# Performance work log

Measured on AMD Instinct MI355X. Metric: run time of the kernel, lower is better.

Reference implementation:

```python
import jax, jax.numpy as jnp
import numpy as np

B, S, HS = 2, 2048, 4096
NH, NKV = 32, 32
HD = HS // NH
INTER = 11008
VOCAB = 32000
EPS = 1e-6
ROPE_BASE = 10000.0


def setup_inputs() -> dict:
    key = jax.random.key(0)
    ks = jax.random.split(key, 16)
    sc = 0.02
    return {
        "hidden_states": jax.random.normal(ks[0], (B, S, HS), jnp.float32),
        "input_ids": jax.random.randint(ks[1], (B, S), 0, VOCAB, jnp.int32),
        "position_ids": jnp.arange(S, dtype=jnp.int32)[None, :],
        "embed": jax.random.normal(ks[2], (VOCAB, HS), jnp.float32) * sc,
        "fc_w": jax.random.normal(ks[3], (HS, 2 * HS), jnp.float32) * sc,
        "fc_b": jnp.zeros((HS,), jnp.float32),
        "q_w": jax.random.normal(ks[4], (NH * HD, HS), jnp.float32) * sc,
        "k_w": jax.random.normal(ks[5], (NKV * HD, HS), jnp.float32) * sc,
        "v_w": jax.random.normal(ks[6], (NKV * HD, HS), jnp.float32) * sc,
        "o_w": jax.random.normal(ks[7], (HS, NH * HD), jnp.float32) * sc,
        "gate_w": jax.random.normal(ks[8], (INTER, HS), jnp.float32) * sc,
        "up_w": jax.random.normal(ks[9], (INTER, HS), jnp.float32) * sc,
        "down_w": jax.random.normal(ks[10], (HS, INTER), jnp.float32) * sc,
        "post_ln_w": jnp.ones((HS,), jnp.float32),
    }


def _rotate_half(x):
    x1, x2 = jnp.split(x, 2, axis=-1)
    return jnp.concatenate((-x2, x1), axis=-1)


def _rms_norm(x, w, eps=EPS):
    x32 = x.astype(jnp.float32)
    x32 = x32 * jax.lax.rsqrt(jnp.mean(x32 * x32, axis=-1, keepdims=True) + eps)
    return (w * x32).astype(x.dtype)


def _forward(hidden_states, input_ids, position_ids, embed, fc_w, fc_b,
             q_w, k_w, v_w, o_w, gate_w, up_w, down_w, post_ln_w):
    # Embedding lookup (detached in original via no_grad)
    embeds = jax.lax.stop_gradient(embed[input_ids])  # [B,S,HS]
    h = jnp.concatenate((embeds, hidden_states), axis=-1) @ fc_w.T + fc_b  # [B,S,HS]

    # --- decoder layer 0 (no input_layernorm) ---
    residual = h
    q = (h @ q_w.T).reshape(B, S, NH, HD).transpose(0, 2, 1, 3)   # [B,NH,S,HD]
    k = (h @ k_w.T).reshape(B, S, NKV, HD).transpose(0, 2, 1, 3)
    v = (h @ v_w.T).reshape(B, S, NKV, HD).transpose(0, 2, 1, 3)

    # RoPE
    pos = position_ids[0].astype(jnp.float32)                      # [S]
    inv_freq = 1.0 / (ROPE_BASE ** (jnp.arange(0, HD, 2, dtype=jnp.float32) / HD))
    freqs = pos[:, None] * inv_freq[None, :]                       # [S,HD/2]
    emb = jnp.concatenate((freqs, freqs), axis=-1)                 # [S,HD]
    cos = jnp.cos(emb)[None, None, :, :]
    sin = jnp.sin(emb)[None, None, :, :]
    q = q * cos + _rotate_half(q) * sin
    k = k * cos + _rotate_half(k) * sin

    # attention (num_kv_groups == 1 here)
    scores = jnp.einsum('bhqd,bhkd->bhqk', q, k) / np.sqrt(HD)     # [B,NH,S,S]
    causal = jnp.triu(jnp.ones((S, S), bool), 1)
    scores = jnp.where(causal[None, None], -jnp.inf, scores)
    attn = jax.nn.softmax(scores.astype(jnp.float32), axis=-1).astype(q.dtype)
    out = jnp.einsum('bhqk,bhkd->bhqd', attn, v)                   # [B,NH,S,HD]
    out = out.transpose(0, 2, 1, 3).reshape(B, S, HS)
    attn_out = out @ o_w.T

    h = residual + attn_out
    residual = h
    hn = _rms_norm(h, post_ln_w)
    mlp = (jax.nn.silu(hn @ gate_w.T) * (hn @ up_w.T)) @ down_w.T
    return residual + mlp


def reference(hidden_states, input_ids, position_ids, embed, fc_w, fc_b,
              q_w, k_w, v_w, o_w, gate_w, up_w, down_w, post_ln_w):
    return _forward(hidden_states, input_ids, position_ids, embed, fc_w, fc_b,
                    q_w, k_w, v_w, o_w, gate_w, up_w, down_w, post_ln_w)
```

## Files before the change

kernel.cpp:

```cpp
#include <hip/hip_runtime.h>
#include <hip/hip_bf16.h>

typedef __attribute__((ext_vector_type(8))) short short8;
typedef __attribute__((ext_vector_type(4))) short short4v;
typedef __attribute__((ext_vector_type(4))) float floatx4;

#define B_SZ 2
#define S_SZ 2048
#define HS_SZ 4096
#define NH_SZ 32
#define HD_SZ 128
#define INTER_SZ 11008
#define M_TOT 4096

__device__ __forceinline__ float b2f(short s){
  unsigned int u = ((unsigned int)(unsigned short)s) << 16;
  return __builtin_bit_cast(float, u);
}
__device__ __forceinline__ short f2b(float f){
  unsigned int u = __builtin_bit_cast(unsigned int, f);
  u = (u + 0x7FFFu + ((u >> 16) & 1u)) >> 16;
  return (short)u;
}

typedef __attribute__((address_space(1))) const unsigned int gu32;
typedef __attribute__((address_space(3))) unsigned int lu32;
__device__ __forceinline__ void gl2lds16(const short* g, short* l){
  __builtin_amdgcn_global_load_lds((gu32*)g, (lu32*)l, 16, 0, 0);
}

#define BARRIER() asm volatile("s_barrier" ::: "memory")
#define WAITV8()  asm volatile("s_waitcnt vmcnt(8)" ::: "memory")
#define WAITV4()  asm volatile("s_waitcnt vmcnt(4)" ::: "memory")
#define WAITV0()  asm volatile("s_waitcnt vmcnt(0)" ::: "memory")

__global__ void cvt_bf16_kernel(const float* __restrict__ src, short* __restrict__ dst, long n8){
  long idx = (long)blockIdx.x * blockDim.x + threadIdx.x;
  if (idx >= n8) return;
  long e = idx * 8;
  floatx4 v0 = *(const floatx4*)(src + e);
  floatx4 v1 = *(const floatx4*)(src + e + 4);
  short8 o;
  o[0]=f2b(v0[0]); o[1]=f2b(v0[1]); o[2]=f2b(v0[2]); o[3]=f2b(v0[3]);
  o[4]=f2b(v1[0]); o[5]=f2b(v1[1]); o[6]=f2b(v1[2]); o[7]=f2b(v1[3]);
  *(short8*)(dst + e) = o;
}

__global__ void embed_concat_kernel(const float* __restrict__ hidden,
                                    const int* __restrict__ ids,
                                    const float* __restrict__ embed,
                                    short* __restrict__ X0){
  long idx = (long)blockIdx.x * blockDim.x + threadIdx.x;
  const long total = (long)M_TOT * (2*HS_SZ) / 4;
  if (idx >= total) return;
  long e = idx * 4;
  int m = (int)(e / (2*HS_SZ));
  int c = (int)(e % (2*HS_SZ));
  const float* src;
  if (c < HS_SZ){
    src = embed + (long)ids[m]*HS_SZ + c;
  } else {
    src = hidden + (long)m*HS_SZ + (c - HS_SZ);
  }
  floatx4 v = *(const floatx4*)src;
  short4v o;
  o[0]=f2b(v[0]); o[1]=f2b(v[1]); o[2]=f2b(v[2]); o[3]=f2b(v[3]);
  *(short4v*)(X0 + e) = o;
}

template<int EPI>
__global__ __launch_bounds__(512, 2)
void gemm256_kernel(const short* __restrict__ A, const short* __restrict__ Bw,
                    int M, int N, int K,
                    const float* __restrict__ bias,
                    const float* __restrict__ resid,
                    short* __restrict__ Cbf,
                    float* __restrict__ Cf){
  __shared__ __align__(16) short lds[65536];
  const int tid = threadIdx.x;
  const int wid = tid >> 6;
  const int lane = tid & 63;
  const int wr = wid >> 2, wc = wid & 3;
  const int lr = lane & 15, lk = lane >> 4;

  const int nwg = gridDim.x * gridDim.y;
  const int id  = blockIdx.y * gridDim.x + blockIdx.x;
  const int cpx = nwg >> 3;
  const int sw  = (id & 7) * cpx + (id >> 3);
  const int bx  = sw % gridDim.x;
  const int by  = sw / gridDim.x;
  const int m0 = bx * 256, n0 = by * 256;

  const int srow = wid*16 + (lane >> 2);
  const int scol = (lane & 3) * 8;
  const short* ga0 = A  + (long)(m0 + srow)*K + scol;
  const short* ga1 = A  + (long)(m0 + 128 + srow)*K + scol;
  const short* gb0 = Bw + (long)(n0 + srow)*K + scol;
  const short* gb1 = Bw + (long)(n0 + 128 + srow)*K + scol;

  floatx4 acc[8][4] = {};
  const int nt = K >> 5;

  auto stage = [&](int t){
    const long kk = (long)t * 32;
    short* db = lds + ((t & 3) * 16384) + wid*512;
    gl2lds16(ga0 + kk, db);
    gl2lds16(ga1 + kk, db + 4096);
    gl2lds16(gb0 + kk, db + 8192);
    gl2lds16(gb1 + kk, db + 12288);
  };

  stage(0); stage(1); stage(2);

  for (int t = 0; t < nt; ++t){
    if (t + 3 < nt) stage(t + 3);
    if (t + 2 < nt)      { WAITV8(); }
    else if (t + 1 < nt) { WAITV4(); }
    else                 { WAITV0(); }
    BARRIER();
    const short* sb = lds + (t & 3) * 16384;
    short8 bfr[4], af[8];
    #pragma unroll
    for (int j=0;j<4;j++) bfr[j] = *(const short8*)(sb + 8192 + (wc*64 + j*16 + lr)*32 + lk*8);
    #pragma unroll
    for (int i=0;i<8;i++) af[i]  = *(const short8*)(sb + (wr*128 + i*16 + lr)*32 + lk*8);
    __builtin_amdgcn_s_setprio(1);
    #pragma unroll
    for (int i=0;i<8;i++)
      #pragma unroll
      for (int j=0;j<4;j++)
        acc[i][j] = __builtin_amdgcn_mfma_f32_16x16x32_bf16(af[i], bfr[j], acc[i][j], 0,0,0);
    __builtin_amdgcn_s_setprio(0);
    BARRIER();
  }

  #pragma unroll
  for (int mf=0; mf<8; mf++){
    #pragma unroll
    for (int nf=0; nf<4; nf++){
      const int col = n0 + wc*64 + nf*16 + lr;
      float bcol = (EPI==1) ? bias[col] : 0.0f;
      #pragma unroll
      for (int r=0; r<4; r++){
        const int row = m0 + wr*128 + mf*16 + lk*4 + r;
        float v = acc[mf][nf][r] + bcol;
        if (EPI==2) v += resid[(long)row*N + col];
        if (EPI==0 || EPI==1) Cbf[(long)row*N + col] = f2b(v);
        if (EPI==1 || EPI==2) Cf[(long)row*N + col] = v;
      }
    }
  }
}

__global__ void rope_kernel(short* __restrict__ q, short* __restrict__ k,
                            const int* __restrict__ pos_ids){
  long idx = (long)blockIdx.x * blockDim.x + threadIdx.x;
  const long total = (long)M_TOT * NH_SZ * (HD_SZ/2);
  if (idx >= total) return;
  int i  = (int)(idx & 63);
  long rh = idx >> 6;
  int h  = (int)(rh & 31);
  int m  = (int)(rh >> 5);
  int s  = m & (S_SZ - 1);
  float p = (float)pos_ids[s];
  const float L2_10000 = 13.28771237954945f;
  float inv = exp2f(-(2.0f*i/(float)HD_SZ) * L2_10000);
  float fr = p * inv;
  float sn, cs;
  sincosf(fr, &sn, &cs);
  long base = (long)m*HS_SZ + h*HD_SZ;
  short* qp = q + base;
  short* kp = k + base;
  float q1=b2f(qp[i]), q2=b2f(qp[i+64]);
  qp[i]    = f2b(q1*cs - q2*sn);
  qp[i+64] = f2b(q2*cs + q1*sn);
  float k1=b2f(kp[i]), k2=b2f(kp[i+64]);
  kp[i]    = f2b(k1*cs - k2*sn);
  kp[i+64] = f2b(k2*cs + k1*sn);
}

__global__ __launch_bounds__(256)
void vtrans_kernel(const short* __restrict__ V, short* __restrict__ VT){
  __shared__ short tile[64][68];
  const int s0 = blockIdx.x * 64;
  const int d0 = blockIdx.y * 64;
  const int bh = blockIdx.z;
  const int b = bh >> 5, h = bh & 31;
  const int tid = threadIdx.x;
  #pragma unroll
  for (int it=0; it<2; it++){
    int e = (it*256 + tid) * 8;
    int ss = e >> 6, col = e & 63;
    short8 v = *(const short8*)(V + ((long)(b*S_SZ + s0 + ss))*HS_SZ + h*HD_SZ + d0 + col);
    #pragma unroll
    for (int j=0;j<8;j++) tile[ss][col+j] = v[j];
  }
  __syncthreads();
  #pragma unroll
  for (int it=0; it<2; it++){
    int e = (it*256 + tid) * 8;
    int dd = e >> 6, scol = e & 63;
    short8 w;
    #pragma unroll
    for (int j=0;j<8;j++) w[j] = tile[scol+j][dd];
    *(short8*)(VT + ((long)(bh*HD_SZ + d0 + dd))*S_SZ + s0 + scol) = w;
  }
}

__global__ __launch_bounds__(256,2)
void attn_kernel(const short* __restrict__ Q, const short* __restrict__ K,
                 const short* __restrict__ VT, short* __restrict__ O){
  constexpr int LPD = 72;
  __shared__ __align__(16) short lds[32768];
  __shared__ __align__(16) short p_lds[4][16*LPD];
  const int bh = blockIdx.y;
  const int b = bh >> 5, h = bh & 31;
  const int q0 = blockIdx.x * 64;
  const int tid = threadIdx.x, wid = tid>>6, lane = tid&63;
  const int lr = lane & 15, lk = lane >> 4;
  const float scale = 0.08838834764831845f;

  const short* qbase = Q + ((long)(b*S_SZ + q0 + wid*16))*HS_SZ + h*HD_SZ;
  short8 qf[4];
  #pragma unroll
  for (int t=0;t<4;t++)
    qf[t] = *(const short8*)(qbase + (long)lr*HS_SZ + t*32 + lk*8);

  const short* kb[4]; const short* vb[4];
  int kloff[4], vloff[4];
  #pragma unroll
  for (int p=0;p<4;p++){
    const int seg = wid*4 + p;
    const int rowk = seg*4 + (lane >> 4);
    const int slotk = (lane & 15) ^ (rowk & 15);
    kb[p] = K + ((long)(b*S_SZ) + rowk)*HS_SZ + h*HD_SZ + slotk*8;
    kloff[p] = seg*512;
    const int dv = seg*8 + (lane >> 3);
    const int slotv = (lane & 7) ^ (dv & 7);
    vb[p] = VT + ((long)(bh*HD_SZ + dv))*S_SZ + slotv*8;
    vloff[p] = 8192 + seg*512;
  }

  floatx4 oacc[8] = {};
  float m_run[4] = {-1e30f,-1e30f,-1e30f,-1e30f};
  float l_run[4] = {0.f,0.f,0.f,0.f};

  const int nt = blockIdx.x + 1;

  #pragma unroll
  for (int p=0;p<4;p++){
    gl2lds16(kb[p], lds + kloff[p]);
    gl2lds16(vb[p], lds + vloff[p]);
  }

  for (int t=0; t<nt; ++t){
    const int dbase = (t & 1) * 16384;
    const int nbase = ((t+1) & 1) * 16384;
    if (t+1 < nt){
      const long kkn = (long)(t+1)*64*HS_SZ;
      const long vkn = (long)(t+1)*64;
      #pragma unroll
      for (int p=0;p<4;p++){
        gl2lds16(kb[p] + kkn, lds + nbase + kloff[p]);
        gl2lds16(vb[p] + vkn, lds + nbase + vloff[p]);
      }
      WAITV8();
    } else {
      WAITV0();
    }
    BARRIER();
    const int kv0 = t*64;
    floatx4 sfr[4];
    #pragma unroll
    for (int fn=0; fn<4; fn++){
      floatx4 s = {0.f,0.f,0.f,0.f};
      const int row = fn*16 + lr;
      #pragma unroll
      for (int tq=0; tq<4; tq++){
        short8 kf = *(const short8*)(lds + dbase + row*128 + (((tq*4+lk)^lr)&15)*8);
        s = __builtin_amdgcn_mfma_f32_16x16x32_bf16(qf[tq], kf, s, 0,0,0);
      }
      sfr[fn] = s;
    }
    float pv[4][4];
    #pragma unroll
    for (int fn=0; fn<4; fn++){
      const int col = kv0 + fn*16 + lr;
      #pragma unroll
      for (int r=0;r<4;r++){
        const int row = q0 + wid*16 + lk*4 + r;
        float sv = sfr[fn][r] * scale;
        pv[fn][r] = (col > row) ? -1e30f : sv;
      }
    }
    float mr4[4];
    int small = 1;
    #pragma unroll
    for (int r=0;r<4;r++){
      float mr = fmaxf(fmaxf(pv[0][r], pv[1][r]), fmaxf(pv[2][r], pv[3][r]));
      mr = fmaxf(mr, __shfl_xor(mr, 1, 16));
      mr = fmaxf(mr, __shfl_xor(mr, 2, 16));
      mr = fmaxf(mr, __shfl_xor(mr, 4, 16));
      mr = fmaxf(mr, __shfl_xor(mr, 8, 16));
      mr4[r] = mr;
      small &= (mr <= m_run[r] + 8.0f) ? 1 : 0;
    }
    const int skip = __all(small);
    float alpha_[4];
    #pragma unroll
    for (int r=0;r<4;r++){
      float mnew = skip ? m_run[r] : fmaxf(m_run[r], mr4[r]);
      alpha_[r] = skip ? 1.0f : __expf(m_run[r] - mnew);
      m_run[r] = mnew;
      float rs = 0.f;
      #pragma unroll
      for (int fn=0; fn<4; fn++){
        float e = __expf(pv[fn][r] - mnew);
        p_lds[wid][(lk*4+r)*LPD + fn*16 + lr] = f2b(e);
        rs += e;
      }
      rs += __shfl_xor(rs, 1, 16);
      rs += __shfl_xor(rs, 2, 16);
      rs += __shfl_xor(rs, 4, 16);
      rs += __shfl_xor(rs, 8, 16);
      l_run[r] = l_run[r]*alpha_[r] + rs;
    }
    if (!skip){
      #pragma unroll
      for (int f=0; f<8; f++){
        #pragma unroll
        for (int r=0;r<4;r++) oacc[f][r] *= alpha_[r];
      }
    }
    short8 pf[2];
    #pragma unroll
    for (int tp=0; tp<2; tp++)
      pf[tp] = *(const short8*)(&p_lds[wid][lr*LPD + tp*32 + lk*8]);
    #pragma unroll
    for (int f=0; f<8; f++){
      const int vrow = f*16 + lr;
      #pragma unroll
      for (int tp=0; tp<2; tp++){
        short8 vf = *(const short8*)(lds + dbase + 8192 + vrow*64 + (((tp*4+lk)^(lr&7))&7)*8);
        oacc[f] = __builtin_amdgcn_mfma_f32_16x16x32_bf16(pf[tp], vf, oacc[f], 0,0,0);
      }
    }
    BARRIER();
  }
  #pragma unroll
  for (int r=0;r<4;r++){
    const float inv = 1.0f / l_run[r];
    const long row = (long)(b*S_SZ + q0 + wid*16 + lk*4 + r);
    #pragma unroll
    for (int f=0; f<8; f++){
      O[row*HS_SZ + h*HD_SZ + f*16 + lr] = f2b(oacc[f][r]*inv);
    }
  }
}

__global__ void rmsnorm_kernel(const float* __restrict__ X, const float* __restrict__ W,
                               short* __restrict__ Y){
  const int row = blockIdx.x;
  const float* x = X + (long)row*HS_SZ;
  float ss = 0.f;
  for (int c = threadIdx.x*4; c < HS_SZ; c += 256*4){
    floatx4 v = *(const floatx4*)(x + c);
    ss += v[0]*v[0] + v[1]*v[1] + v[2]*v[2] + v[3]*v[3];
  }
  ss += __shfl_xor(ss, 32); ss += __shfl_xor(ss, 16);
  ss += __shfl_xor(ss, 8);  ss += __shfl_xor(ss, 4);
  ss += __shfl_xor(ss, 2);  ss += __shfl_xor(ss, 1);
  __shared__ float red[4];
  if ((threadIdx.x & 63) == 0) red[threadIdx.x >> 6] = ss;
  __syncthreads();
  ss = red[0] + red[1] + red[2] + red[3];
  const float rs = rsqrtf(ss / (float)HS_SZ + 1e-6f);
  for (int c = threadIdx.x*4; c < HS_SZ; c += 256*4){
    floatx4 v = *(const floatx4*)(x + c);
    floatx4 w = *(const floatx4*)(W + c);
    short4v o;
    o[0]=f2b(v[0]*rs*w[0]); o[1]=f2b(v[1]*rs*w[1]);
    o[2]=f2b(v[2]*rs*w[2]); o[3]=f2b(v[3]*rs*w[3]);
    *(short4v*)(Y + (long)row*HS_SZ + c) = o;
  }
}

__global__ void silu_mul_kernel(short* __restrict__ G, const short* __restrict__ U){
  long idx = (long)blockIdx.x * blockDim.x + threadIdx.x;
  const long total = (long)M_TOT * INTER_SZ / 8;
  if (idx >= total) return;
  long e = idx * 8;
  short8 g = *(short8*)(G + e);
  short8 u = *(const short8*)(U + e);
  short8 o;
  #pragma unroll
  for (int j=0;j<8;j++){
    float gf = b2f(g[j]);
    float uf = b2f(u[j]);
    float s = gf / (1.0f + __expf(-gf));
    o[j] = f2b(s * uf);
  }
  *(short8*)(G + e) = o;
}

extern "C" void kernel_launch(void* const* d_in, const int* in_sizes, int n_in,
                              void* d_out, int out_size, void* d_ws, size_t ws_size,
                              hipStream_t stream){
  (void)in_sizes; (void)n_in; (void)out_size;
  const float* hidden = (const float*)d_in[0];
  const int*   ids    = (const int*)d_in[1];
  const int*   pos    = (const int*)d_in[2];
  const float* embed  = (const float*)d_in[3];
  const float* fc_w   = (const float*)d_in[4];
  const float* fc_b   = (const float*)d_in[5];
  const float* q_w    = (const float*)d_in[6];
  const float* k_w    = (const float*)d_in[7];
  const float* v_w    = (const float*)d_in[8];
  const float* o_w    = (const float*)d_in[9];
  const float* gate_w = (const float*)d_in[10];
  const float* up_w   = (const float*)d_in[11];
  const float* down_w = (const float*)d_in[12];
  const float* ln_w   = (const float*)d_in[13];

  char* ws = (char*)d_ws;
  size_t off = 0;
  auto alloc = [&](size_t bytes)->char*{
    char* p = ws + off;
    off = (off + bytes + 255) & ~(size_t)255;
    return p;
  };
  short* wbf  = (short*)alloc((size_t)INTER_SZ*HS_SZ*2);
  short* X0   = (short*)alloc((size_t)M_TOT*2*HS_SZ*2);
  short* h_bf = (short*)alloc((size_t)M_TOT*HS_SZ*2);
  float* h_f  = (float*)alloc((size_t)M_TOT*HS_SZ*4);
  short* q_bf = (short*)alloc((size_t)M_TOT*HS_SZ*2);
  short* k_bf = (short*)alloc((size_t)M_TOT*HS_SZ*2);
  short* v_bf = (short*)alloc((size_t)M_TOT*HS_SZ*2);
  short* vt_bf= (short*)alloc((size_t)M_TOT*HS_SZ*2);
  short* a_bf = (short*)alloc((size_t)M_TOT*HS_SZ*2);
  float* h2_f = (float*)alloc((size_t)M_TOT*HS_SZ*4);
  short* hn_bf= (short*)alloc((size_t)M_TOT*HS_SZ*2);
  short* g_bf = (short*)alloc((size_t)M_TOT*INTER_SZ*2);
  short* u_bf = (short*)alloc((size_t)M_TOT*INTER_SZ*2);
  if (ws_size < off) return;

  auto cvt = [&](const float* src, short* dst, long n){
    long n8 = n / 8;
    cvt_bf16_kernel<<<(int)((n8 + 255)/256), 256, 0, stream>>>(src, dst, n8);
  };

  embed_concat_kernel<<<32768, 256, 0, stream>>>(hidden, ids, embed, X0);

  cvt(fc_w, wbf, (long)HS_SZ*2*HS_SZ);
  gemm256_kernel<1><<<dim3(16,16), 512, 0, stream>>>(X0, wbf, M_TOT, HS_SZ, 2*HS_SZ,
                                                     fc_b, nullptr, h_bf, h_f);
  cvt(q_w, wbf, (long)HS_SZ*HS_SZ);
  gemm256_kernel<0><<<dim3(16,16), 512, 0, stream>>>(h_bf, wbf, M_TOT, HS_SZ, HS_SZ,
                                                     nullptr, nullptr, q_bf, nullptr);
  cvt(k_w, wbf, (long)HS_SZ*HS_SZ);
  gemm256_kernel<0><<<dim3(16,16), 512, 0, stream>>>(h_bf, wbf, M_TOT, HS_SZ, HS_SZ,
                                                     nullptr, nullptr, k_bf, nullptr);
  cvt(v_w, wbf, (long)HS_SZ*HS_SZ);
  gemm256_kernel<0><<<dim3(16,16), 512, 0, stream>>>(h_bf, wbf, M_TOT, HS_SZ, HS_SZ,
                                                     nullptr, nullptr, v_bf, nullptr);
  rope_kernel<<<32768, 256, 0, stream>>>(q_bf, k_bf, pos);
  vtrans_kernel<<<dim3(S_SZ/64, HD_SZ/64, B_SZ*NH_SZ), 256, 0, stream>>>(v_bf, vt_bf);
  attn_kernel<<<dim3(S_SZ/64, B_SZ*NH_SZ), 256, 0, stream>>>(q_bf, k_bf, vt_bf, a_bf);
  cvt(o_w, wbf, (long)HS_SZ*HS_SZ);
  gemm256_kernel<2><<<dim3(16,16), 512, 0, stream>>>(a_bf, wbf, M_TOT, HS_SZ, HS_SZ,
                                                     nullptr, h_f, nullptr, h2_f);
  rmsnorm_kernel<<<M_TOT, 256, 0, stream>>>(h2_f, ln_w, hn_bf);
  cvt(gate_w, wbf, (long)INTER_SZ*HS_SZ);
  gemm256_kernel<0><<<dim3(16,43), 512, 0, stream>>>(hn_bf, wbf, M_TOT, INTER_SZ, HS_SZ,
                                                     nullptr, nullptr, g_bf, nullptr);
  cvt(up_w, wbf, (long)INTER_SZ*HS_SZ);
  gemm256_kernel<0><<<dim3(16,43), 512, 0, stream>>>(hn_bf, wbf, M_TOT, INTER_SZ, HS_SZ,
                                                     nullptr, nullptr, u_bf, nullptr);
  silu_mul_kernel<<<22016, 256, 0, stream>>>(g_bf, u_bf);
  cvt(down_w, wbf, (long)HS_SZ*INTER_SZ);
  gemm256_kernel<2><<<dim3(16,16), 512, 0, stream>>>(g_bf, wbf, M_TOT, HS_SZ, INTER_SZ,
                                                     nullptr, h2_f, nullptr, (float*)d_out);
}
```

Measured before the change: 2.689 ms.

## Restructure GEMM mainloop into 8-wave ping-pong with K=64 tiles and swizzled LDS

Rewrites the 256x256 bf16 GEMM main loop to use K=64 tiles with double buffering, split into four 128x128 quadrants. Each quadrant's MFMA block is interleaved with a global-to-LDS stage of the next tile, with barriers in between. LDS rows are XOR-swizzled to avoid bank conflicts on the 64-wide rows. The aim is to overlap memory loads with MFMA work and cut LDS conflicts, at the cost of more barriers and tighter vmcnt bookkeeping that could break correctness or stall waves.

```diff
diff --git a/kernel.cpp b/kernel.cpp
--- a/kernel.cpp
+++ b/kernel.cpp
@@ -32,6 +32,7 @@
 #define BARRIER() asm volatile("s_barrier" ::: "memory")
 #define WAITV8()  asm volatile("s_waitcnt vmcnt(8)" ::: "memory")
 #define WAITV4()  asm volatile("s_waitcnt vmcnt(4)" ::: "memory")
+#define WAITV2()  asm volatile("s_waitcnt vmcnt(2)" ::: "memory")
 #define WAITV0()  asm volatile("s_waitcnt vmcnt(0)" ::: "memory")
 
 __global__ void cvt_bf16_kernel(const float* __restrict__ src, short* __restrict__ dst, long n8){
@@ -68,6 +69,35 @@
   *(short4v*)(X0 + e) = o;
 }
 
+#define G_STAGE(op,h,kof,qb) { \
+  gl2lds16(gs[op][h] + (kof), lds + (qb) + (op)*16384 + (h)*8192 + wid*1024); \
+  gl2lds16(gs[op][h] + k8 + (kof), lds + (qb) + (op)*16384 + (h)*8192 + wid*1024 + 512); }
+
+#define LD_A(Mh,pb) { \
+  _Pragma("unroll") \
+  for (int mf=0; mf<4; mf++) \
+    _Pragma("unroll") \
+    for (int ks=0; ks<2; ks++) \
+      af[mf][ks] = *(const short8*)(lds + (pb) + ((Mh)*128 + wr2*64 + mf*16 + lr)*64 + (((ks*4+lk)^lr7))*8); }
+
+#define LD_B(BB,Nh,pb) { \
+  _Pragma("unroll") \
+  for (int nf=0; nf<2; nf++) \
+    _Pragma("unroll") \
+    for (int ks=0; ks<2; ks++) \
+      BB[nf][ks] = *(const short8*)(lds + (pb) + 16384 + ((Nh)*128 + wc2*32 + nf*16 + lr)*64 + (((ks*4+lk)^lr7))*8); }
+
+#define MMQ(Mh,Nh,BB) { \
+  __builtin_amdgcn_s_setprio(1); \
+  _Pragma("unroll") \
+  for (int mf=0; mf<4; mf++) \
+    _Pragma("unroll") \
+    for (int nf=0; nf<2; nf++){ \
+      acc[Mh][Nh][mf][nf] = __builtin_amdgcn_mfma_f32_16x16x32_bf16(af[mf][0], BB[nf][0], acc[Mh][Nh][mf][nf], 0,0,0); \
+      acc[Mh][Nh][mf][nf] = __builtin_amdgcn_mfma_f32_16x16x32_bf16(af[mf][1], BB[nf][1], acc[Mh][Nh][mf][nf], 0,0,0); \
+    } \
+  __builtin_amdgcn_s_setprio(0); }
+
 template<int EPI>
 __global__ __launch_bounds__(512, 2)
 void gemm256_kernel(const short* __restrict__ A, const short* __restrict__ Bw,
@@ -80,8 +110,9 @@
   const int tid = threadIdx.x;
   const int wid = tid >> 6;
   const int lane = tid & 63;
-  const int wr = wid >> 2, wc = wid & 3;
+  const int wr2 = wid >> 2, wc2 = wid & 3;
   const int lr = lane & 15, lk = lane >> 4;
+  const int lr7 = lr & 7;
 
   const int nwg = gridDim.x * gridDim.y;
   const int id  = blockIdx.y * gridDim.x + blockIdx.x;
@@ -91,62 +122,82 @@
   const int by  = sw / gridDim.x;
   const int m0 = bx * 256, n0 = by * 256;
 
-  const int srow = wid*16 + (lane >> 2);
-  const int scol = (lane & 3) * 8;
-  const short* ga0 = A  + (long)(m0 + srow)*K + scol;
-  const short* ga1 = A  + (long)(m0 + 128 + srow)*K + scol;
-  const short* gb0 = Bw + (long)(n0 + srow)*K + scol;
-  const short* gb1 = Bw + (long)(n0 + 128 + srow)*K + scol;
-
-  floatx4 acc[8][4] = {};
-  const int nt = K >> 5;
-
-  auto stage = [&](int t){
-    const long kk = (long)t * 32;
-    short* db = lds + ((t & 3) * 16384) + wid*512;
-    gl2lds16(ga0 + kk, db);
-    gl2lds16(ga1 + kk, db + 4096);
-    gl2lds16(gb0 + kk, db + 8192);
-    gl2lds16(gb1 + kk, db + 12288);
-  };
-
-  stage(0); stage(1); stage(2);
-
-  for (int t = 0; t < nt; ++t){
-    if (t + 3 < nt) stage(t + 3);
-    if (t + 2 < nt)      { WAITV8(); }
-    else if (t + 1 < nt) { WAITV4(); }
-    else                 { WAITV0(); }
-    BARRIER();
-    const short* sb = lds + (t & 3) * 16384;
-    short8 bfr[4], af[8];
-    #pragma unroll
-    for (int j=0;j<4;j++) bfr[j] = *(const short8*)(sb + 8192 + (wc*64 + j*16 + lr)*32 + lk*8);
-    #pragma unroll
-    for (int i=0;i<8;i++) af[i]  = *(const short8*)(sb + (wr*128 + i*16 + lr)*32 + lk*8);
-    __builtin_amdgcn_s_setprio(1);
-    #pragma unroll
-    for (int i=0;i<8;i++)
-      #pragma unroll
-      for (int j=0;j<4;j++)
-        acc[i][j] = __builtin_amdgcn_mfma_f32_16x16x32_bf16(af[i], bfr[j], acc[i][j], 0,0,0);
-    __builtin_amdgcn_s_setprio(0);
-    BARRIER();
-  }
-
-  #pragma unroll
-  for (int mf=0; mf<8; mf++){
-    #pragma unroll
-    for (int nf=0; nf<4; nf++){
-      const int col = n0 + wc*64 + nf*16 + lr;
-      float bcol = (EPI==1) ? bias[col] : 0.0f;
-      #pragma unroll
-      for (int r=0; r<4; r++){
-        const int row = m0 + wr*128 + mf*16 + lk*4 + r;
-        float v = acc[mf][nf][r] + bcol;
-        if (EPI==2) v += resid[(long)row*N + col];
-        if (EPI==0 || EPI==1) Cbf[(long)row*N + col] = f2b(v);
-        if (EPI==1 || EPI==2) Cf[(long)row*N + col] = v;
+  const int srow = lane >> 3;
+  const int sslot = (lane & 7) ^ srow;
+  const long k8 = 8L * K;
+  const short* gs[2][2];
+  #pragma unroll
+  for (int op=0; op<2; op++)
+    #pragma unroll
+    for (int h=0; h<2; h++){
+      const int row = (op ? n0 : m0) + h*128 + wid*16 + srow;
+      gs[op][h] = (op ? Bw : A) + (long)row*K + sslot*8;
+    }
+
+  floatx4 acc[2][2][4][2] = {};
+  short8 af[4][2], b0[2][2], b1[2][2];
+  const int nt = K >> 6;
+
+  G_STAGE(0,0,0,0); G_STAGE(1,0,0,0); G_STAGE(1,1,0,0); G_STAGE(0,1,0,0);
+  WAITV4(); BARRIER();
+
+  for (int t = 0; t < nt-1; ++t){
+    const int pb = (t & 1) << 15;
+    const int qb = pb ^ 32768;
+    const long kof = (long)(t+1) * 64;
+    LD_A(0,pb); LD_B(b0,0,pb);
+    G_STAGE(0,0,kof,qb);
+    BARRIER();
+    MMQ(0,0,b0);
+    WAITV4(); BARRIER();
+    LD_B(b1,1,pb);
+    G_STAGE(1,0,kof,qb);
+    BARRIER();
+    MMQ(0,1,b1);
+    WAITV4(); BARRIER();
+    LD_A(1,pb);
+    G_STAGE(1,1,kof,qb);
+    BARRIER();
+    MMQ(1,1,b1);
+    BARRIER();
+    G_STAGE(0,1,kof,qb);
+    BARRIER();
+    MMQ(1,0,b0);
+    WAITV4(); BARRIER();
+  }
+  {
+    const int pb = ((nt-1) & 1) << 15;
+    LD_A(0,pb); LD_B(b0,0,pb);
+    BARRIER(); MMQ(0,0,b0);
+    WAITV2(); BARRIER();
+    LD_B(b1,1,pb);
+    BARRIER(); MMQ(0,1,b1);
+    WAITV0(); BARRIER();
+    LD_A(1,pb);
+    BARRIER(); MMQ(1,1,b1);
+    BARRIER();
+    MMQ(1,0,b0);
+  }
+
+  #pragma unroll
+  for (int Mh=0; Mh<2; Mh++){
+    #pragma unroll
+    for (int Nh=0; Nh<2; Nh++){
+      #pragma unroll
+      for (int mf=0; mf<4; mf++){
+        #pragma unroll
+        for (int nf=0; nf<2; nf++){
+          const int col = n0 + Nh*128 + wc2*32 + nf*16 + lr;
+          float bcol = (EPI==1) ? bias[col] : 0.0f;
+          #pragma unroll
+          for (int r=0; r<4; r++){
+            const int row = m0 + Mh*128 + wr2*64 + mf*16 + lk*4 + r;
+            float v = acc[Mh][Nh][mf][nf][r] + bcol;
+            if (EPI==2) v += resid[(long)row*N + col];
+            if (EPI==0 || EPI==1) Cbf[(long)row*N + col] = f2b(v);
+            if (EPI==1 || EPI==2) Cf[(long)row*N + col] = v;
+          }
+        }
       }
     }
   }
```

New measurement: 2.279 ms. 1.18x faster.
